# Kernel tuning notes

Measured on AMD Instinct MI355X. Metric: run time of the kernel, lower is better.

## Reference

```python
import jax, jax.numpy as jnp
import numpy as np

N_EMBEDS = 1024
N_HEADS = 16
EPS = 1e-3


def layer_norm(x, gamma, beta):
    mean = jnp.mean(x, axis=-1, keepdims=True)
    var = jnp.mean((x - mean) ** 2, axis=-1, keepdims=True)
    return gamma * (x - mean) / jnp.sqrt(var + EPS) + beta


def setup_inputs() -> dict:
    key = jax.random.key(0)
    ks = jax.random.split(key, 8)
    B, T, C = 4, 2048, N_EMBEDS
    s = 1.0 / np.sqrt(C)
    return {
        "x": jax.random.normal(ks[0], (B, T, C), dtype=jnp.float32),
        "w_qkv": jax.random.normal(ks[1], (C, 3 * C), dtype=jnp.float32) * s,
        "w_proj": jax.random.normal(ks[2], (C, C), dtype=jnp.float32) * s,
        "b_proj": jnp.zeros((C,), dtype=jnp.float32),
        "w1": jax.random.normal(ks[3], (C, 4 * C), dtype=jnp.float32) * s,
        "b1": jnp.zeros((4 * C,), dtype=jnp.float32),
        "w2": jax.random.normal(ks[4], (4 * C, C), dtype=jnp.float32) * (0.5 / np.sqrt(C)),
        "b2": jnp.zeros((C,), dtype=jnp.float32),
        "gamma1": jnp.ones((C,), dtype=jnp.float32),
        "beta1": jnp.zeros((C,), dtype=jnp.float32),
        "gamma2": jnp.ones((C,), dtype=jnp.float32),
        "beta2": jnp.zeros((C,), dtype=jnp.float32),
    }


def reference(x, w_qkv, w_proj, b_proj, w1, b1, w2, b2, gamma1, beta1, gamma2, beta2):
    B, T, C = x.shape
    H = N_HEADS
    D = C // H
    scale = D ** -0.5

    # --- attention sub-layer (pre-LN) ---
    h = layer_norm(x, gamma1, beta1)
    qkv = h @ w_qkv                      # [B,T,3C]
    q, k, v = jnp.split(qkv, 3, axis=-1)
    q = q.reshape(B, T, H, D).transpose(0, 2, 1, 3)  # [B,H,T,D]
    k = k.reshape(B, T, H, D).transpose(0, 2, 1, 3)
    v = v.reshape(B, T, H, D).transpose(0, 2, 1, 3)
    att = jnp.einsum('bhqd,bhkd->bhqk', q, k) * scale
    causal = jnp.tril(jnp.ones((T, T), dtype=bool))
    att = jnp.where(causal[None, None], att, jnp.float32(-1e9))
    att = jax.nn.softmax(att, axis=-1)
    out = jnp.einsum('bhqk,bhkd->bhqd', att, v)
    out = out.transpose(0, 2, 1, 3).reshape(B, T, C)
    x = x + out @ w_proj + b_proj

    # --- FFN sub-layer (pre-LN, erf-GELU) ---
    h = layer_norm(x, gamma2, beta2)
    h = jax.nn.gelu(h @ w1 + b1, approximate=False)
    x = x + h @ w2 + b2
    return x
```

## Files before the change

kernel.cpp:

```cpp
#include <hip/hip_runtime.h>
#include <hip/hip_bf16.h>
#include <cstdint>
#include <cstddef>

#define B_ 4
#define T_ 2048
#define C_ 1024
#define H_ 16
#define D_ 64
#define M_ (B_*T_)

using bf16_t = __hip_bfloat16;
typedef __bf16 v8bf __attribute__((ext_vector_type(8)));
typedef float  v4f  __attribute__((ext_vector_type(4)));
typedef float  f32x16 __attribute__((ext_vector_type(16)));

#define QSCALE (0.125f * 1.44269504088896340736f)

static __device__ __forceinline__ bf16_t f2bf(float v){ return __float2bfloat16(v); }
static __device__ __forceinline__ float bfraw2f(unsigned short u){
  union { unsigned int i; float f; } c; c.i = ((unsigned int)u) << 16; return c.f;
}

static __device__ __forceinline__ void glds16(const bf16_t* g, bf16_t* l){
  __builtin_amdgcn_global_load_lds((__attribute__((address_space(1))) void*)g,
                                   (__attribute__((address_space(3))) void*)l, 16, 0, 0);
}

static __device__ __forceinline__ uint32_t cvt_pk_bf16(float lo, float hi){
  uint32_t w;
  asm("v_cvt_pk_bf16_f32 %0, %1, %2" : "=v"(w) : "v"(lo), "v"(hi));
  return w;
}

static __device__ __forceinline__ float gelu_fast(float x){
  const float u = __builtin_fmaf(0.044715f * x * x, x, x);
  const float e = __builtin_amdgcn_exp2f(2.3021256637f * u);
  return x - x * __builtin_amdgcn_rcpf(1.0f + e);
}

__global__ __launch_bounds__(256)
void k_prep(const float* __restrict__ in0, bf16_t* __restrict__ out0,
            const float* __restrict__ in1, bf16_t* __restrict__ out1,
            const float* __restrict__ in2, bf16_t* __restrict__ out2,
            const float* __restrict__ in3, bf16_t* __restrict__ out3,
            const float* __restrict__ x,  const float* __restrict__ gamma,
            const float* __restrict__ beta, bf16_t* __restrict__ hb){
  const int bid = blockIdx.x;
  const int tid = threadIdx.x;
  if (bid < 12288) {
    __shared__ float tile[32][33];
    const float* in; bf16_t* out; int K, N, lb;
    if (bid < 3072)      { in=in0; out=out0; K=1024; N=3072; lb=bid; }
    else if (bid < 4096) { in=in1; out=out1; K=1024; N=1024; lb=bid-3072; }
    else if (bid < 8192) { in=in2; out=out2; K=1024; N=4096; lb=bid-4096; }
    else                 { in=in3; out=out3; K=4096; N=1024; lb=bid-8192; }
    const int nbx = N >> 5;
    const int k0 = (lb / nbx) * 32, n0 = (lb % nbx) * 32;
    const int tx = tid & 31, ty = tid >> 5;
    #pragma unroll
    for(int j=0;j<32;j+=8) tile[ty+j][tx] = in[(size_t)(k0+ty+j)*N + n0+tx];
    __syncthreads();
    #pragma unroll
    for(int j=0;j<32;j+=8) out[(size_t)(n0+ty+j)*K + k0+tx] = f2bf(tile[tx][ty+j]);
  } else {
    const int row = bid - 12288;
    const float4 v = reinterpret_cast<const float4*>(x + (size_t)row*C_)[tid];
    float s  = v.x+v.y+v.z+v.w;
    float ss = v.x*v.x+v.y*v.y+v.z*v.z+v.w*v.w;
    #pragma unroll
    for(int m=1;m<64;m<<=1){ s += __shfl_xor(s,m); ss += __shfl_xor(ss,m); }
    __shared__ float sbuf[4], ssbuf[4];
    const int wid = tid>>6, lane = tid&63;
    if(lane==0){ sbuf[wid]=s; ssbuf[wid]=ss; }
    __syncthreads();
    s  = sbuf[0]+sbuf[1]+sbuf[2]+sbuf[3];
    ss = ssbuf[0]+ssbuf[1]+ssbuf[2]+ssbuf[3];
    const float mean = s * (1.0f/C_);
    const float var  = ss * (1.0f/C_) - mean*mean;
    const float rstd = rsqrtf(var + 1e-3f);
    const float4 g = reinterpret_cast<const float4*>(gamma)[tid];
    const float4 b = reinterpret_cast<const float4*>(beta)[tid];
    union { ushort4 u; bf16_t h[4]; } pk;
    pk.h[0] = f2bf(g.x*(v.x-mean)*rstd + b.x);
    pk.h[1] = f2bf(g.y*(v.y-mean)*rstd + b.y);
    pk.h[2] = f2bf(g.z*(v.z-mean)*rstd + b.z);
    pk.h[3] = f2bf(g.w*(v.w-mean)*rstd + b.w);
    *reinterpret_cast<ushort4*>(hb + (size_t)row*C_ + tid*4) = pk.u;
  }
}

__global__ __launch_bounds__(256) void k_layernorm(const float* __restrict__ x,
                                                   const float* __restrict__ gamma,
                                                   const float* __restrict__ beta,
                                                   bf16_t* __restrict__ out){
  int row = blockIdx.x;
  int tid = threadIdx.x;
  const float4 v = reinterpret_cast<const float4*>(x + (size_t)row*C_)[tid];
  float s  = v.x+v.y+v.z+v.w;
  float ss = v.x*v.x+v.y*v.y+v.z*v.z+v.w*v.w;
  #pragma unroll
  for(int m=1;m<64;m<<=1){ s += __shfl_xor(s,m); ss += __shfl_xor(ss,m); }
  __shared__ float sbuf[4], ssbuf[4];
  int wid = tid>>6, lane = tid&63;
  if(lane==0){ sbuf[wid]=s; ssbuf[wid]=ss; }
  __syncthreads();
  s  = sbuf[0]+sbuf[1]+sbuf[2]+sbuf[3];
  ss = ssbuf[0]+ssbuf[1]+ssbuf[2]+ssbuf[3];
  float mean = s * (1.0f/C_);
  float var  = ss * (1.0f/C_) - mean*mean;
  float rstd = rsqrtf(var + 1e-3f);
  const float4 g = reinterpret_cast<const float4*>(gamma)[tid];
  const float4 b = reinterpret_cast<const float4*>(beta)[tid];
  union { ushort4 u; bf16_t h[4]; } pk;
  pk.h[0] = f2bf(g.x*(v.x-mean)*rstd + b.x);
  pk.h[1] = f2bf(g.y*(v.y-mean)*rstd + b.y);
  pk.h[2] = f2bf(g.z*(v.z-mean)*rstd + b.z);
  pk.h[3] = f2bf(g.w*(v.w-mean)*rstd + b.w);
  *reinterpret_cast<ushort4*>(out + (size_t)row*C_ + tid*4) = pk.u;
}

__global__ __launch_bounds__(256)
void k_add2(const bf16_t* __restrict__ p0, const bf16_t* __restrict__ p1,
            const float* __restrict__ bias, float* out){
  const int row = blockIdx.x, tid = threadIdx.x;
  float4 xr = reinterpret_cast<const float4*>(out + (size_t)row*C_)[tid];
  const ushort4 a = reinterpret_cast<const ushort4*>(p0 + (size_t)row*C_)[tid];
  const ushort4 b = reinterpret_cast<const ushort4*>(p1 + (size_t)row*C_)[tid];
  const float4 g = reinterpret_cast<const float4*>(bias)[tid];
  xr.x += bfraw2f(a.x) + bfraw2f(b.x) + g.x;
  xr.y += bfraw2f(a.y) + bfraw2f(b.y) + g.y;
  xr.z += bfraw2f(a.z) + bfraw2f(b.z) + g.z;
  xr.w += bfraw2f(a.w) + bfraw2f(b.w) + g.w;
  reinterpret_cast<float4*>(out + (size_t)row*C_)[tid] = xr;
}

template<int MODE>
__global__ __launch_bounds__(512, 1)
void k_gemm9(const bf16_t* __restrict__ A, const bf16_t* __restrict__ Bt,
             const float* __restrict__ bias, const float* resid,
             void* out0, void* out1, void* out2,
             int N, int ld, int klen, int gx, int tc)
{
  __shared__ __align__(16) bf16_t As[2][2][128*64];
  __shared__ __align__(16) bf16_t Bs[2][2][128*64];
  const int tid = threadIdx.x, lane = tid & 63, w = tid >> 6;
  const int wm = w >> 2, wn = w & 3;
  const int koff = blockIdx.z * klen;

  const int sswz = ((lane & 7) ^ ((lane >> 3) & 7)) * 8;
  const int srow = w * 8 + (lane >> 3);

  int row0, col0;
  const bf16_t *Agb, *Bgb;
  auto set_tile = [&](int tile){
    const int swz = (tile & 7) * (tc >> 3) + (tile >> 3);
    const int ct = swz % gx, rt = swz / gx;
    row0 = rt * 256; col0 = ct * 256;
    Agb = A  + (size_t)(row0 + srow) * ld + koff + sswz;
    Bgb = Bt + (size_t)(col0 + srow) * ld + koff + sswz;
  };

  auto stageA = [&](int tt, int hh){
    const bf16_t* src = Agb + (size_t)(hh * 128) * ld + tt * 64;
    bf16_t* dst = &As[tt & 1][hh][w * 512];
    glds16(src, dst);
    glds16(src + (size_t)64 * ld, dst + 4096);
  };
  auto stageB = [&](int tt, int hh){
    const bf16_t* src = Bgb + (size_t)(hh * 128) * ld + tt * 64;
    bf16_t* dst = &Bs[tt & 1][hh][w * 512];
    glds16(src, dst);
    glds16(src + (size_t)64 * ld, dst + 4096);
  };
  auto stage_prologue = [&](){
    stageA(0,0); stageA(0,1); stageB(0,0); stageB(0,1);
    stageB(1,0); stageB(1,1); stageA(1,0);
  };

  v8bf af[4][2], bfv[4][2];
  v4f acc[8][4];

  auto LDA = [&](int bb, int mh){
    const bf16_t* base = &As[bb][wm][0];
    #pragma unroll
    for (int m = 0; m < 4; ++m)
      #pragma unroll
      for (int kk = 0; kk < 2; ++kk) {
        const int r  = mh*64 + m*16 + (lane & 15);
        const int sl = (kk*4 + (lane >> 4)) ^ (lane & 7);
        af[m][kk] = *reinterpret_cast<const v8bf*>(base + r*64 + sl*8);
      }
  };
  auto LDB4 = [&](int bb, int nh){
    const bf16_t* base = &Bs[bb][wn >> 1][0];
    #pragma unroll
    for (int n = 0; n < 2; ++n)
      #pragma unroll
      for (int kk = 0; kk < 2; ++kk) {
        const int r  = (wn & 1)*64 + (nh*2+n)*16 + (lane & 15);
        const int sl = (kk*4 + (lane >> 4)) ^ (lane & 7);
        bfv[nh*2+n][kk] = *reinterpret_cast<const v8bf*>(base + r*64 + sl*8);
      }
  };

#define MFMA_Q(mh_, nh_) \
  __builtin_amdgcn_s_setprio(1); \
  _Pragma("unroll") \
  for (int kk = 0; kk < 2; ++kk) \
    _Pragma("unroll") \
    for (int m = 0; m < 4; ++m) \
      _Pragma("unroll") \
      for (int n = 0; n < 2; ++n) \
        acc[(mh_)*4+m][(nh_)*2+n] = __builtin_amdgcn_mfma_f32_16x16x32_bf16( \
            af[m][kk], bfv[(nh_)*2+n][kk], acc[(mh_)*4+m][(nh_)*2+n], 0,0,0); \
  __builtin_amdgcn_s_setprio(0);

#define BAR()   __builtin_amdgcn_s_barrier()
#define LGKM0() do { asm volatile("s_waitcnt lgkmcnt(0)" ::: "memory"); \
                     __builtin_amdgcn_sched_barrier(0); } while(0)

  const int NP = (klen >> 6) >> 1;
  int tile = blockIdx.x;
  set_tile(tile);
  stage_prologue();

  for (;;) {
    asm volatile("s_waitcnt vmcnt(6)" ::: "memory");
    BAR();
    #pragma unroll
    for (int mf = 0; mf < 8; ++mf)
      #pragma unroll
      for (int nf = 0; nf < 4; ++nf)
        acc[mf][nf] = (v4f){0.f, 0.f, 0.f, 0.f};

    for (int j = 0; j < NP; ++j) {
      const int t2 = 2*j + 2, t3 = 2*j + 3;
      const bool more = (j + 1 < NP);
      LDA(0, 0); LDB4(0, 0);
      stageA(2*j + 1, 1);
      BAR(); LGKM0(); MFMA_Q(0, 0); BAR();
      LDB4(0, 1);
      if (more) stageB(t2, 0);
      BAR(); LGKM0(); MFMA_Q(0, 1); BAR();
      LDA(0, 1);
      if (more) stageB(t2, 1);
      BAR(); LGKM0(); MFMA_Q(1, 0); BAR();
      if (more) { stageA(t2, 0); asm volatile("s_waitcnt vmcnt(6)" ::: "memory"); }
      else      {                asm volatile("s_waitcnt vmcnt(0)" ::: "memory"); }
      BAR(); MFMA_Q(1, 1); BAR();
      LDA(1, 0); LDB4(1, 0);
      if (more) stageA(t2, 1);
      BAR(); LGKM0(); MFMA_Q(0, 0); BAR();
      LDB4(1, 1);
      if (more) stageB(t3, 0);
      BAR(); LGKM0(); MFMA_Q(0, 1); BAR();
      LDA(1, 1);
      if (more) stageB(t3, 1);
      BAR(); LGKM0(); MFMA_Q(1, 0); BAR();
      if (more) { stageA(t3, 0); asm volatile("s_waitcnt vmcnt(6)" ::: "memory"); }
      else      {                asm volatile("s_waitcnt vmcnt(0)" ::: "memory"); }
      BAR(); MFMA_Q(1, 1); BAR();
    }

    const int erow0 = row0, ecol0 = col0;
    const int next = tile + (int)gridDim.x;
    const bool have_next = (next < tc);
    if (have_next) { set_tile(next); stage_prologue(); }

    #pragma unroll
    for (int mf = 0; mf < 8; ++mf) {
      const int rbase = erow0 + wm*128 + mf*16 + (lane>>4)*4;
      #pragma unroll
      for (int nf = 0; nf < 4; ++nf) {
        const int c = ecol0 + wn*64 + nf*16 + (lane&15);
        #pragma unroll
        for (int i = 0; i < 4; ++i) {
          const int rr = rbase + i;
          float v = acc[mf][nf][i];
          if constexpr(MODE==0){
            const int sec = c >> 10, cc = c & 1023;
            const int h = cc >> 6, d = cc & 63;
            const int b = rr >> 11, t = rr & 2047;
            if(sec==0)      ((bf16_t*)out0)[((size_t)(b*H_ + h)*T_ + t)*D_ + d] = f2bf(v * QSCALE);
            else if(sec==1) ((bf16_t*)out1)[((size_t)(b*H_ + h)*T_ + t)*D_ + d] = f2bf(v);
            else            ((bf16_t*)out2)[((size_t)(b*H_ + h)*D_ + d)*T_ + t] = f2bf(v);
          } else if constexpr(MODE==2){
            ((bf16_t*)out0)[(size_t)rr*N + c] = f2bf(gelu_fast(v + bias[c]));
          } else {
            bf16_t* dst = blockIdx.z ? (bf16_t*)out1 : (bf16_t*)out0;
            dst[(size_t)rr*N + c] = f2bf(v);
          }
        }
      }
    }
    if (!have_next) break;
    tile = next;
  }
#undef MFMA_Q
#undef BAR
#undef LGKM0
}

__global__ __launch_bounds__(512, 1)
void k_gemm8(const bf16_t* __restrict__ A, const bf16_t* __restrict__ Bt,
             const float* __restrict__ bias, const float* resid,
             float* out0, int N, int K, int gx)
{
  __shared__ __align__(16) bf16_t As[2][256*64];
  __shared__ __align__(16) bf16_t Bs[3][128*64];
  const int tid = threadIdx.x, lane = tid & 63, w = tid >> 6;
  const int wm = w >> 1, wn = w & 1;

  const int nwg = gx * 32;
  const int orig = blockIdx.y * gx + blockIdx.x;
  const int swz = (orig & 7) * (nwg >> 3) + (orig >> 3);
  const int ct = swz % gx, rt = swz / gx;
  const int row0 = rt * 256, col0 = ct * 128;

  const int sswz = ((lane & 7) ^ ((lane >> 3) & 7)) * 8;
  const int srow = w * 8 + (lane >> 3);
  const bf16_t* Agb = A  + (size_t)(row0 + srow) * K + sswz;
  const bf16_t* Bgb = Bt + (size_t)(col0 + srow) * K + sswz;

  auto stageA = [&](int tt){
    const bf16_t* src = Agb + tt * 64;
    bf16_t* dst = &As[tt & 1][w * 512];
    #pragma unroll
    for (int i = 0; i < 4; ++i)
      glds16(src + (size_t)(i*64) * K, dst + i*4096);
  };
  auto stageB = [&](int tt){
    const bf16_t* src = Bgb + tt * 64;
    bf16_t* dst = &Bs[tt % 3][w * 512];
    #pragma unroll
    for (int i = 0; i < 2; ++i)
      glds16(src + (size_t)(i*64) * K, dst + i*4096);
  };

  v8bf af[4][2], bfv[4][2];
  v4f acc[4][4] = {};

  auto LDA = [&](int ab){
    const bf16_t* base = &As[ab][0];
    #pragma unroll
    for (int m = 0; m < 4; ++m)
      #pragma unroll
      for (int kk = 0; kk < 2; ++kk) {
        const int r  = wm*64 + m*16 + (lane & 15);
        const int sl = (kk*4 + (lane >> 4)) ^ (lane & 7);
        af[m][kk] = *reinterpret_cast<const v8bf*>(base + r*64 + sl*8);
      }
  };
  auto LDB = [&](int bb, int nh){
    const bf16_t* base = &Bs[bb][0];
    #pragma unroll
    for (int n = 0; n < 2; ++n)
      #pragma unroll
      for (int kk = 0; kk < 2; ++kk) {
        const int r  = wn*64 + (nh*2+n)*16 + (lane & 15);
        const int sl = (kk*4 + (lane >> 4)) ^ (lane & 7);
        bfv[nh*2+n][kk] = *reinterpret_cast<const v8bf*>(base + r*64 + sl*8);
      }
  };

#define MFMA_Q(nh_) \
  __builtin_amdgcn_s_setprio(1); \
  _Pragma("unroll") \
  for (int kk = 0; kk < 2; ++kk) \
    _Pragma("unroll") \
    for (int m = 0; m < 4; ++m) \
      _Pragma("unroll") \
      for (int n = 0; n < 2; ++n) \
        acc[m][(nh_)*2+n] = __builtin_amdgcn_mfma_f32_16x16x32_bf16( \
            af[m][kk], bfv[(nh_)*2+n][kk], acc[m][(nh_)*2+n], 0,0,0); \
  __builtin_amdgcn_s_setprio(0);

#define BAR()   __builtin_amdgcn_s_barrier()
#define LGKM0() do { asm volatile("s_waitcnt lgkmcnt(0)" ::: "memory"); \
                     __builtin_amdgcn_sched_barrier(0); } while(0)
#define VM6()   asm volatile("s_waitcnt vmcnt(6)" ::: "memory")
#define VM0()   asm volatile("s_waitcnt vmcnt(0)" ::: "memory")

  const int NP = (K >> 6) >> 1;
  stageB(0); stageA(0); stageB(1); stageA(1);
  VM6();
  BAR();

  for (int j = 0; j < NP; ++j) {
    const int t0 = 2*j, t1 = 2*j + 1, t2 = 2*j + 2, t3 = 2*j + 3;
    const bool more = (j + 1 < NP);
    LDA(0); LDB(t0 % 3, 0);
    if (more) stageB(t2);
    BAR(); LGKM0(); MFMA_Q(0); BAR();
    LDB(t0 % 3, 1);
    if (more) { stageA(t2); VM6(); } else { VM0(); }
    BAR(); LGKM0(); MFMA_Q(1); BAR();
    LDA(1); LDB(t1 % 3, 0);
    if (more) stageB(t3);
    BAR(); LGKM0(); MFMA_Q(0); BAR();
    LDB(t1 % 3, 1);
    if (more) { stageA(t3); VM6(); } else { VM0(); }
    BAR(); LGKM0(); MFMA_Q(1); BAR();
  }
#undef MFMA_Q
#undef BAR
#undef LGKM0
#undef VM6
#undef VM0

  #pragma unroll
  for (int mf = 0; mf < 4; ++mf) {
    const int rbase = row0 + wm*64 + mf*16 + (lane>>4)*4;
    #pragma unroll
    for (int nf = 0; nf < 4; ++nf) {
      const int c = col0 + wn*64 + nf*16 + (lane&15);
      #pragma unroll
      for (int i = 0; i < 4; ++i) {
        const int rr = rbase + i;
        out0[(size_t)rr*N + c] = acc[mf][nf][i] + bias[c] + resid[(size_t)rr*N + c];
      }
    }
  }
}

__global__ __launch_bounds__(256)
void k_attn(const bf16_t* __restrict__ Q, const bf16_t* __restrict__ Kg,
            const bf16_t* __restrict__ Vt, bf16_t* __restrict__ O)
{
  __shared__ __align__(16) bf16_t Ks [64][72];
  __shared__ __align__(16) bf16_t Vts[64][72];
  __shared__ __align__(16) bf16_t Os [128][72];
  const int bh = blockIdx.y;
  const int pair = blockIdx.x;
  const int tid = threadIdx.x, lane = tid & 63, w = tid >> 6;
  const int ql = lane & 31, hi = lane >> 5;
  const int srow = tid >> 2;
  const int scol = (tid & 3) * 16;
  const bf16_t* Kgp = Kg + ((size_t)bh*T_ + srow)*D_ + scol;
  const bf16_t* Vtp = Vt + ((size_t)bh*D_ + srow)*T_ + scol;
  const int b = bh >> 4, h = bh & 15;

  for(int half=0; half<2; ++half){
    const int qt = half ? pair : (15 - pair);
    const int qbase = qt*128 + w*32;
    const int q = qbase + ql;

    v8bf qf[4];
    {
      const bf16_t* Qb = Q + ((size_t)bh*T_ + q)*D_ + hi*8;
      #pragma unroll
      for(int ds=0; ds<4; ds++)
        qf[ds] = *reinterpret_cast<const v8bf*>(Qb + ds*16);
    }

    f32x16 accO[2] = {};
    float mrun = -1e30f, lrun = 0.0f;
    const int NT = (qt + 1) * 2;

    v8bf kr0 = *reinterpret_cast<const v8bf*>(Kgp);
    v8bf kr1 = *reinterpret_cast<const v8bf*>(Kgp + 8);
    v8bf vr0 = *reinterpret_cast<const v8bf*>(Vtp);
    v8bf vr1 = *reinterpret_cast<const v8bf*>(Vtp + 8);

    for(int t=0; t<NT; t++){
      const int kv0 = t*64;
      *reinterpret_cast<v8bf*>(&Ks [srow][scol  ]) = kr0;
      *reinterpret_cast<v8bf*>(&Ks [srow][scol+8]) = kr1;
      *reinterpret_cast<v8bf*>(&Vts[srow][scol  ]) = vr0;
      *reinterpret_cast<v8bf*>(&Vts[srow][scol+8]) = vr1;
      __syncthreads();
      if(t+1 < NT){
        const size_t kn = (size_t)(kv0 + 64);
        kr0 = *reinterpret_cast<const v8bf*>(Kgp + kn*D_);
        kr1 = *reinterpret_cast<const v8bf*>(Kgp + kn*D_ + 8);
        vr0 = *reinterpret_cast<const v8bf*>(Vtp + kn);
        vr1 = *reinterpret_cast<const v8bf*>(Vtp + kn + 8);
      }

      if(kv0 <= qbase + 31){
        f32x16 sT[2] = {};
        __builtin_amdgcn_s_setprio(1);
        #pragma unroll
        for(int kvh=0; kvh<2; kvh++)
          #pragma unroll
          for(int ds=0; ds<4; ds++){
            v8bf kf = *reinterpret_cast<const v8bf*>(&Ks[kvh*32 + ql][ds*16 + hi*8]);
            sT[kvh] = __builtin_amdgcn_mfma_f32_32x32x16_bf16(kf, qf[ds], sT[kvh], 0,0,0);
          }
        __builtin_amdgcn_s_setprio(0);

        if(kv0 + 63 > qbase){
          const int qrel = q - kv0 - hi*4;
          #pragma unroll
          for(int kvh=0; kvh<2; kvh++)
            #pragma unroll
            for(int r=0; r<16; r++){
              const int c = kvh*32 + (r&3) + 8*(r>>2);
              if(c > qrel) sT[kvh][r] = -1e30f;
            }
        }

        float pm = sT[0][0];
        #pragma unroll
        for(int r=1; r<16; r++) pm = fmaxf(pm, sT[0][r]);
        #pragma unroll
        for(int r=0; r<16; r++) pm = fmaxf(pm, sT[1][r]);
        pm = fmaxf(pm, __shfl_xor(pm, 32));

        if(__any(pm - mrun > 8.0f)){
          const float mnew = fmaxf(mrun, pm);
          const float corr = __builtin_amdgcn_exp2f(mrun - mnew);
          mrun = mnew;
          lrun *= corr;
          #pragma unroll
          for(int dh=0; dh<2; dh++)
            #pragma unroll
            for(int r=0; r<16; r++) accO[dh][r] *= corr;
        }

        float rs = 0.0f;
        #pragma unroll
        for(int kvh=0; kvh<2; kvh++)
          #pragma unroll
          for(int r=0; r<16; r++){
            float p = __builtin_amdgcn_exp2f(sT[kvh][r] - mrun);
            sT[kvh][r] = p;
            rs += p;
          }
        rs += __shfl_xor(rs, 32);
        lrun += rs;

        v8bf pfrag[4];
        #pragma unroll
        for(int s4=0; s4<4; s4++){
          const int kvh = s4>>1, bb = (s4&1)*8;
          uint32_t wa = cvt_pk_bf16(sT[kvh][bb+0], sT[kvh][bb+1]);
          uint32_t wb = cvt_pk_bf16(sT[kvh][bb+2], sT[kvh][bb+3]);
          uint32_t wc = cvt_pk_bf16(sT[kvh][bb+4], sT[kvh][bb+5]);
          uint32_t wd = cvt_pk_bf16(sT[kvh][bb+6], sT[kvh][bb+7]);
          uint32_t xwa = (uint32_t)__shfl_xor((int)wa, 32);
          uint32_t xwb = (uint32_t)__shfl_xor((int)wb, 32);
          uint32_t xwc = (uint32_t)__shfl_xor((int)wc, 32);
          uint32_t xwd = (uint32_t)__shfl_xor((int)wd, 32);
          union { uint32_t u[4]; v8bf v; } pk;
          pk.u[0] = hi ? xwc : wa;
          pk.u[1] = hi ? xwd : wb;
          pk.u[2] = hi ? wc  : xwa;
          pk.u[3] = hi ? wd  : xwb;
          pfrag[s4] = pk.v;
        }

        __builtin_amdgcn_s_setprio(1);
        #pragma unroll
        for(int dh=0; dh<2; dh++)
          #pragma unroll
          for(int s4=0; s4<4; s4++){
            v8bf vf = *reinterpret_cast<const v8bf*>(&Vts[dh*32 + ql][s4*16 + hi*8]);
            accO[dh] = __builtin_amdgcn_mfma_f32_32x32x16_bf16(vf, pfrag[s4], accO[dh], 0,0,0);
          }
        __builtin_amdgcn_s_setprio(0);
      }
      __syncthreads();
    }

    const float inv = 1.0f / lrun;
    #pragma unroll
    for(int dh=0; dh<2; dh++)
      #pragma unroll
      for(int rg=0; rg<4; rg++){
        uint32_t lo_ = cvt_pk_bf16(accO[dh][rg*4+0]*inv, accO[dh][rg*4+1]*inv);
        uint32_t hi_ = cvt_pk_bf16(accO[dh][rg*4+2]*inv, accO[dh][rg*4+3]*inv);
        uint2 w2; w2.x = lo_; w2.y = hi_;
        *reinterpret_cast<uint2*>(&Os[w*32 + ql][dh*32 + rg*8 + hi*4]) = w2;
      }
    __syncthreads();
    const int orow = tid >> 1, ocol = (tid & 1) * 32;
    bf16_t* Og = O + ((size_t)(b*T_ + qt*128 + orow))*C_ + h*64 + ocol;
    #pragma unroll
    for(int j=0;j<4;j++)
      *reinterpret_cast<v8bf*>(Og + j*8) = *reinterpret_cast<const v8bf*>(&Os[orow][ocol + j*8]);
    __syncthreads();
  }
}

extern "C" void kernel_launch(void* const* d_in, const int* in_sizes, int n_in,
                              void* d_out, int out_size, void* d_ws, size_t ws_size,
                              hipStream_t stream) {
  const float* x      = (const float*)d_in[0];
  const float* w_qkv  = (const float*)d_in[1];
  const float* w_proj = (const float*)d_in[2];
  const float* b_proj = (const float*)d_in[3];
  const float* w1     = (const float*)d_in[4];
  const float* b1     = (const float*)d_in[5];
  const float* w2     = (const float*)d_in[6];
  const float* b2     = (const float*)d_in[7];
  const float* gamma1 = (const float*)d_in[8];
  const float* beta1  = (const float*)d_in[9];
  const float* gamma2 = (const float*)d_in[10];
  const float* beta2  = (const float*)d_in[11];

  char* ws = (char*)d_ws;
  bf16_t* wqkv_t  = (bf16_t*)(ws + 0);
  bf16_t* wproj_t = (bf16_t*)(ws + 6291456);
  bf16_t* w1_t    = (bf16_t*)(ws + 8388608);
  bf16_t* w2_t    = (bf16_t*)(ws + 16777216);
  bf16_t* qb      = (bf16_t*)(ws + 25165824);
  bf16_t* kb      = (bf16_t*)(ws + 41943040);
  bf16_t* vtb     = (bf16_t*)(ws + 58720256);
  bf16_t* obuf    = (bf16_t*)(ws + 75497472);
  bf16_t* hb      = (bf16_t*)(ws + 92274688);
  bf16_t* gb      = (bf16_t*)(ws + 25165824);
  float*  x2      = (float*)d_out;

  k_prep<<<20480, 256, 0, stream>>>(w_qkv, wqkv_t, w_proj, wproj_t,
                                    w1, w1_t, w2, w2_t,
                                    x, gamma1, beta1, hb);

  k_gemm9<0><<<dim3(256, 1, 1), 512, 0, stream>>>(hb, wqkv_t, nullptr, nullptr,
                                                  qb, kb, vtb, 3072, 1024, 1024, 12, 384);
  k_attn<<<dim3(8, B_*H_), 256, 0, stream>>>(qb, kb, vtb, obuf);

  k_gemm8<<<dim3(8, 32), 512, 0, stream>>>(obuf, wproj_t, b_proj, x,
                                           x2, 1024, 1024, 8);
  k_layernorm<<<M_, 256, 0, stream>>>(x2, gamma2, beta2, hb);

  k_gemm9<2><<<dim3(256, 1, 1), 512, 0, stream>>>(hb, w1_t, b1, nullptr,
                                                  gb, nullptr, nullptr, 4096, 1024, 1024, 16, 512);
  k_gemm9<4><<<dim3(128, 1, 2), 512, 0, stream>>>(gb, w2_t, nullptr, nullptr,
                                                  obuf, hb, nullptr, 1024, 4096, 2048, 4, 128);
  k_add2<<<M_, 256, 0, stream>>>(obuf, hb, b2, x2);
}
```

Measured before the change: 367.5 us.

## Double-buffer LDS fragment registers to overlap LDS reads with MFMA

Splits the A and B register fragments into two ping-pong sets, so the LDS reads for the next quadrant are issued before the current quadrant's MFMAs instead of waiting on lgkmcnt(0) with a sched barrier. The aim is to hide LDS read latency behind matrix-core work in the 256x256 GEMM main loop. This costs more VGPRs and depends on the compiler inserting the correct lgkmcnt waits, since the explicit waits are gone. The prefetch into the next iteration crosses barriers and buffer reuse, which adds hazard risk.

Result: slower. 515.0 us (+40.1%).

```diff
diff --git a/kernel.cpp b/kernel.cpp
--- a/kernel.cpp
+++ b/kernel.cpp
@@ -178,10 +178,11 @@
     stageB(1,0); stageB(1,1); stageA(1,0);
   };
 
-  v8bf af[4][2], bfv[4][2];
+  v8bf afA[4][2], afB[4][2];
+  v8bf bfA[2][2], bfB[2][2];
   v4f acc[8][4];
 
-  auto LDA = [&](int bb, int mh){
+  auto LDA_TO = [&](v8bf (&dst)[4][2], int bb, int mh){
     const bf16_t* base = &As[bb][wm][0];
     #pragma unroll
     for (int m = 0; m < 4; ++m)
@@ -189,10 +190,10 @@
       for (int kk = 0; kk < 2; ++kk) {
         const int r  = mh*64 + m*16 + (lane & 15);
         const int sl = (kk*4 + (lane >> 4)) ^ (lane & 7);
-        af[m][kk] = *reinterpret_cast<const v8bf*>(base + r*64 + sl*8);
-      }
-  };
-  auto LDB4 = [&](int bb, int nh){
+        dst[m][kk] = *reinterpret_cast<const v8bf*>(base + r*64 + sl*8);
+      }
+  };
+  auto LDB_TO = [&](v8bf (&dst)[2][2], int bb, int nh){
     const bf16_t* base = &Bs[bb][wn >> 1][0];
     #pragma unroll
     for (int n = 0; n < 2; ++n)
@@ -200,11 +201,11 @@
       for (int kk = 0; kk < 2; ++kk) {
         const int r  = (wn & 1)*64 + (nh*2+n)*16 + (lane & 15);
         const int sl = (kk*4 + (lane >> 4)) ^ (lane & 7);
-        bfv[nh*2+n][kk] = *reinterpret_cast<const v8bf*>(base + r*64 + sl*8);
-      }
-  };
-
-#define MFMA_Q(mh_, nh_) \
+        dst[n][kk] = *reinterpret_cast<const v8bf*>(base + r*64 + sl*8);
+      }
+  };
+
+#define MFMA_X(AF, BF, mh_, nh_) \
   __builtin_amdgcn_s_setprio(1); \
   _Pragma("unroll") \
   for (int kk = 0; kk < 2; ++kk) \
@@ -213,12 +214,12 @@
       _Pragma("unroll") \
       for (int n = 0; n < 2; ++n) \
         acc[(mh_)*4+m][(nh_)*2+n] = __builtin_amdgcn_mfma_f32_16x16x32_bf16( \
-            af[m][kk], bfv[(nh_)*2+n][kk], acc[(mh_)*4+m][(nh_)*2+n], 0,0,0); \
+            AF[m][kk], BF[n][kk], acc[(mh_)*4+m][(nh_)*2+n], 0,0,0); \
   __builtin_amdgcn_s_setprio(0);
 
 #define BAR()   __builtin_amdgcn_s_barrier()
-#define LGKM0() do { asm volatile("s_waitcnt lgkmcnt(0)" ::: "memory"); \
-                     __builtin_amdgcn_sched_barrier(0); } while(0)
+#define VM6()   asm volatile("s_waitcnt vmcnt(6)" ::: "memory")
+#define VM0()   asm volatile("s_waitcnt vmcnt(0)" ::: "memory")
 
   const int NP = (klen >> 6) >> 1;
   int tile = blockIdx.x;
@@ -226,41 +227,57 @@
   stage_prologue();
 
   for (;;) {
-    asm volatile("s_waitcnt vmcnt(6)" ::: "memory");
+    VM6();
     BAR();
     #pragma unroll
     for (int mf = 0; mf < 8; ++mf)
       #pragma unroll
       for (int nf = 0; nf < 4; ++nf)
         acc[mf][nf] = (v4f){0.f, 0.f, 0.f, 0.f};
+
+    LDA_TO(afA, 0, 0); LDB_TO(bfA, 0, 0);
 
     for (int j = 0; j < NP; ++j) {
       const int t2 = 2*j + 2, t3 = 2*j + 3;
       const bool more = (j + 1 < NP);
-      LDA(0, 0); LDB4(0, 0);
       stageA(2*j + 1, 1);
-      BAR(); LGKM0(); MFMA_Q(0, 0); BAR();
-      LDB4(0, 1);
+      BAR();
+      LDB_TO(bfB, 0, 1);
+      MFMA_X(afA, bfA, 0, 0);
+      BAR();
       if (more) stageB(t2, 0);
-      BAR(); LGKM0(); MFMA_Q(0, 1); BAR();
-      LDA(0, 1);
+      BAR();
+      LDA_TO(afB, 0, 1);
+      MFMA_X(afA, bfB, 0, 1);
+      BAR();
       if (more) stageB(t2, 1);
-      BAR(); LGKM0(); MFMA_Q(1, 0); BAR();
-      if (more) { stageA(t2, 0); asm volatile("s_waitcnt vmcnt(6)" ::: "memory"); }
-      else      {                asm volatile("s_waitcnt vmcnt(0)" ::: "memory"); }
-      BAR(); MFMA_Q(1, 1); BAR();
-      LDA(1, 0); LDB4(1, 0);
+      BAR();
+      MFMA_X(afB, bfA, 1, 0);
+      BAR();
+      if (more) { stageA(t2, 0); VM6(); } else { VM0(); }
+      BAR();
+      LDA_TO(afA, 1, 0); LDB_TO(bfA, 1, 0);
+      MFMA_X(afB, bfB, 1, 1);
+      BAR();
       if (more) stageA(t2, 1);
-      BAR(); LGKM0(); MFMA_Q(0, 0); BAR();
-      LDB4(1, 1);
+      BAR();
+      LDB_TO(bfB, 1, 1);
+      MFMA_X(afA, bfA, 0, 0);
+      BAR();
       if (more) stageB(t3, 0);
-      BAR(); LGKM0(); MFMA_Q(0, 1); BAR();
-      LDA(1, 1);
+      BAR();
+      LDA_TO(afB, 1, 1);
+      MFMA_X(afA, bfB, 0, 1);
+      BAR();
       if (more) stageB(t3, 1);
-      BAR(); LGKM0(); MFMA_Q(1, 0); BAR();
-      if (more) { stageA(t3, 0); asm volatile("s_waitcnt vmcnt(6)" ::: "memory"); }
-      else      {                asm volatile("s_waitcnt vmcnt(0)" ::: "memory"); }
-      BAR(); MFMA_Q(1, 1); BAR();
+      BAR();
+      MFMA_X(afB, bfA, 1, 0);
+      BAR();
+      if (more) { stageA(t3, 0); VM6(); } else { VM0(); }
+      BAR();
+      if (more) { LDA_TO(afA, 0, 0); LDB_TO(bfA, 0, 0); }
+      MFMA_X(afB, bfB, 1, 1);
+      BAR();
     }
 
     const int erow0 = row0, ecol0 = col0;
@@ -297,9 +314,10 @@
     if (!have_next) break;
     tile = next;
   }
-#undef MFMA_Q
+#undef MFMA_X
 #undef BAR
-#undef LGKM0
+#undef VM6
+#undef VM0
 }
 
 __global__ __launch_bounds__(512, 1)
```
